# Performance work log

Measured on AMD Instinct MI355X. Metric: run time of the kernel, lower is better.

## Reference

```python
import jax, jax.numpy as jnp
import numpy as np

N_NODES = 50000
N_EDGES = 800000
LN_EPS = 1e-5


def setup_inputs() -> dict:
    key = jax.random.key(0)
    ks = jax.random.split(key, 6)
    B, N, D = 2, N_NODES, 128
    x = jax.random.normal(ks[0], (B, N, D), dtype=jnp.float32)
    A_rows = jax.random.randint(ks[1], (N_EDGES,), 0, N, dtype=jnp.int32)
    A_cols = jax.random.randint(ks[2], (N_EDGES,), 0, N, dtype=jnp.int32)
    A_vals = jax.random.uniform(ks[3], (N_EDGES,), dtype=jnp.float32)
    W = jax.random.normal(ks[4], (D, D), dtype=jnp.float32) * (1.0 / np.sqrt(D))
    b = jnp.zeros((D,), dtype=jnp.float32)
    gamma = jnp.ones((D,), dtype=jnp.float32)
    beta = jnp.zeros((D,), dtype=jnp.float32)
    return {"x": x, "A_rows": A_rows, "A_cols": A_cols, "A_vals": A_vals,
            "W": W, "b": b, "gamma": gamma, "beta": beta}


def reference(x, A_rows, A_cols, A_vals, W, b, gamma, beta):
    B, N, D = x.shape
    # SpMM: A @ x2 where x2 = x.transpose(0,1).reshape(N, B*D)
    x2 = jnp.transpose(x, (1, 0, 2)).reshape(N, B * D)  # [N, B*D]
    msgs = x2[A_cols] * A_vals[:, None]                 # [E, B*D]
    y2 = jax.ops.segment_sum(msgs, A_rows, num_segments=N)  # [N, B*D]
    out = jnp.transpose(y2.reshape(N, B, D), (1, 0, 2))  # [B, N, D]
    # Linear -> LayerNorm -> GELU (dropout = identity in eval)
    h = out @ W + b
    mu = jnp.mean(h, axis=-1, keepdims=True)
    var = jnp.var(h, axis=-1, keepdims=True)
    h = (h - mu) * jax.lax.rsqrt(var + LN_EPS) * gamma + beta
    return jax.nn.gelu(h, approximate=False)
```

## Files before the change

### kernel.cpp

```cpp
#include <hip/hip_runtime.h>
#include <hip/hip_fp16.h>
#include <cstdint>
#include <cstddef>

#define N_NODES 50000
#define N_EDGES 800000
#define D 128
#define M_ROWS (2 * N_NODES)
#define N_TILES (M_ROWS / 16)
#define LN_EPS 1e-5f

typedef __attribute__((ext_vector_type(8))) short bf16x8;
typedef __attribute__((ext_vector_type(4))) float f32x4;

__device__ inline unsigned short bf16_rne(float f) {
  unsigned u = __float_as_uint(f);
  unsigned r = (u + 0x7FFFu + ((u >> 16) & 1u)) >> 16;
  return (unsigned short)r;
}

__global__ __launch_bounds__(256) void k_prep(const float* __restrict__ W,
                                              unsigned short* __restrict__ wt_hi,
                                              unsigned short* __restrict__ wt_lo,
                                              const int* __restrict__ rows,
                                              int* __restrict__ offs) {
  int b = blockIdx.x;
  if (b < 64) {
    int i = b * 256 + threadIdx.x;
    int d = i >> 7, j = i & 127;
    float v = W[i];
    unsigned short hb = bf16_rne(v);
    float rem = v - __uint_as_float((unsigned)hb << 16);
    wt_hi[j * 128 + d] = hb;
    wt_lo[j * 128 + d] = bf16_rne(rem);
  } else {
    int e = (b - 64) * 256 + threadIdx.x;
    if (e < N_EDGES) atomicAdd(&offs[rows[e]], 1);
  }
}

__global__ __launch_bounds__(1024) void k_scan1(int* __restrict__ offs,
                                                int* __restrict__ bsum) {
  __shared__ int s[1024];
  int tid = threadIdx.x;
  int i = blockIdx.x * 1024 + tid;
  int v = (i < N_NODES) ? offs[i] : 0;
  s[tid] = v;
  __syncthreads();
  for (int o = 1; o < 1024; o <<= 1) {
    int t = (tid >= o) ? s[tid - o] : 0;
    __syncthreads();
    s[tid] += t;
    __syncthreads();
  }
  if (i < N_NODES) offs[i] = s[tid] - v;
  if (tid == 1023) bsum[blockIdx.x] = s[tid];
}

__global__ void k_scan2(int* __restrict__ bsum, int nb) {
  if (threadIdx.x == 0) {
    int run = 0;
    for (int b = 0; b < nb; b++) { int t = bsum[b]; bsum[b] = run; run += t; }
  }
}

__global__ __launch_bounds__(1024) void k_scan3(int* __restrict__ offs,
                                                const int* __restrict__ bsum) {
  int i = blockIdx.x * 1024 + threadIdx.x;
  if (i < N_NODES) offs[i] += bsum[blockIdx.x];
}

__global__ __launch_bounds__(256) void k_scatter(const int* __restrict__ rows,
                                                 const int* __restrict__ cols,
                                                 const float* __restrict__ vals,
                                                 int* __restrict__ offs,
                                                 int2* __restrict__ epair) {
  int e = blockIdx.x * 256 + threadIdx.x;
  if (e < N_EDGES) {
    int r = rows[e];
    int pos = atomicAdd(&offs[r], 1);
    int2 p; p.x = cols[e]; p.y = __float_as_int(vals[e]);
    epair[pos] = p;
  }
}

__global__ __launch_bounds__(512) void k_gemm_z(const float* __restrict__ x,
                                                const unsigned short* __restrict__ wt_hi,
                                                const unsigned short* __restrict__ wt_lo,
                                                __half* __restrict__ z) {
  __shared__ unsigned short lw[2][128 * 128];
  int tid = threadIdx.x;

  for (int c = tid; c < 2048; c += 512) {
    int j = c >> 4;
    int k16 = c & 15;
    int soff = j * 256 + ((k16 * 16) ^ ((j & 7) << 4));
    *reinterpret_cast<float4*>(reinterpret_cast<char*>(lw[0]) + soff) =
        *reinterpret_cast<const float4*>(wt_hi + j * 128 + k16 * 8);
    *reinterpret_cast<float4*>(reinterpret_cast<char*>(lw[1]) + soff) =
        *reinterpret_cast<const float4*>(wt_lo + j * 128 + k16 * 8);
  }

  int wave = tid >> 6, l = tid & 63;
  int tile = blockIdx.x * 8 + wave;
  bool active = tile < N_TILES;
  int lrow = l & 15;
  int kg = l >> 4;

  float4 xv[4][2];
  if (active) {
    const float* xr = x + (size_t)(tile * 16 + lrow) * D + kg * 8;
#pragma unroll
    for (int kc = 0; kc < 4; kc++) {
      xv[kc][0] = *reinterpret_cast<const float4*>(xr + kc * 32);
      xv[kc][1] = *reinterpret_cast<const float4*>(xr + kc * 32 + 4);
    }
  } else {
#pragma unroll
    for (int kc = 0; kc < 4; kc++) {
      xv[kc][0] = float4{0.f, 0.f, 0.f, 0.f};
      xv[kc][1] = float4{0.f, 0.f, 0.f, 0.f};
    }
  }
  __syncthreads();

  bf16x8 ahi[4], alo[4];
#pragma unroll
  for (int kc = 0; kc < 4; kc++) {
    float tmp[8];
    *reinterpret_cast<float4*>(&tmp[0]) = xv[kc][0];
    *reinterpret_cast<float4*>(&tmp[4]) = xv[kc][1];
    bf16x8 h, lo8;
#pragma unroll
    for (int e = 0; e < 8; e++) {
      unsigned short hb = bf16_rne(tmp[e]);
      float rem = tmp[e] - __uint_as_float((unsigned)hb << 16);
      h[e] = (short)hb;
      lo8[e] = (short)bf16_rne(rem);
    }
    ahi[kc] = h; alo[kc] = lo8;
  }

  f32x4 acc[8];
#pragma unroll
  for (int jt = 0; jt < 8; jt++) acc[jt] = (f32x4){0.f, 0.f, 0.f, 0.f};

#pragma unroll
  for (int kc = 0; kc < 4; kc++) {
#pragma unroll
    for (int jt = 0; jt < 8; jt++) {
      int j = jt * 16 + lrow;
      int kbyte = kc * 64 + kg * 16;
      int soff = j * 256 + (kbyte ^ ((j & 7) << 4));
      bf16x8 bhi = *reinterpret_cast<bf16x8*>(reinterpret_cast<char*>(lw[0]) + soff);
      bf16x8 blo = *reinterpret_cast<bf16x8*>(reinterpret_cast<char*>(lw[1]) + soff);
      acc[jt] = __builtin_amdgcn_mfma_f32_16x16x32_bf16(ahi[kc], bhi, acc[jt], 0, 0, 0);
      acc[jt] = __builtin_amdgcn_mfma_f32_16x16x32_bf16(alo[kc], bhi, acc[jt], 0, 0, 0);
      acc[jt] = __builtin_amdgcn_mfma_f32_16x16x32_bf16(ahi[kc], blo, acc[jt], 0, 0, 0);
    }
  }

  __syncthreads();
  unsigned short* lds = &lw[0][0] + (size_t)wave * 2176;
  int rbase = kg * 4;
#pragma unroll
  for (int jt = 0; jt < 8; jt++) {
#pragma unroll
    for (int r = 0; r < 4; r++) {
      __half hv = __float2half(acc[jt][r]);
      lds[(rbase + r) * 136 + jt * 16 + lrow] = __half_as_ushort(hv);
    }
  }
  __syncthreads();
  if (active) {
    const char* ldsb = reinterpret_cast<const char*>(lds);
#pragma unroll
    for (int r = 0; r < 16; r++) {
      unsigned v = *reinterpret_cast<const unsigned*>(ldsb + r * 272 + 4 * l);
      *reinterpret_cast<unsigned*>(&z[(size_t)(tile * 16 + r) * D + 2 * l]) = v;
    }
  }
}

__device__ inline float gelu_exact(float v) {
  return 0.5f * v * (1.0f + erff(v * 0.70710678118654752440f));
}

__global__ __launch_bounds__(256) void k_spmm_ln(const __half* __restrict__ z,
                                                 const int* __restrict__ offs,
                                                 const int2* __restrict__ epair,
                                                 const float* __restrict__ bias,
                                                 const float* __restrict__ gamma,
                                                 const float* __restrict__ beta,
                                                 float* __restrict__ out) {
  int r = blockIdx.x * 4 + (threadIdx.x >> 6);
  int l = threadIdx.x & 63;
  int start = (r == 0) ? 0 : offs[r - 1];
  int end = offs[r];

  float2 a0 = {0.f, 0.f}, a1 = {0.f, 0.f};
  const __half* z1 = z + (size_t)N_NODES * D;

  int k = start;
  for (; k + 1 < end; k += 2) {
    int2 e0 = epair[k];
    int2 e1 = epair[k + 1];
    size_t b0 = (size_t)e0.x * D + 2 * l;
    size_t b1 = (size_t)e1.x * D + 2 * l;
    float v0 = __int_as_float(e0.y);
    float v1 = __int_as_float(e1.y);
    float2 f00 = __half22float2(*reinterpret_cast<const __half2*>(&z[b0]));
    float2 f01 = __half22float2(*reinterpret_cast<const __half2*>(&z1[b0]));
    float2 f10 = __half22float2(*reinterpret_cast<const __half2*>(&z[b1]));
    float2 f11 = __half22float2(*reinterpret_cast<const __half2*>(&z1[b1]));
    a0.x += v0 * f00.x; a0.y += v0 * f00.y;
    a1.x += v0 * f01.x; a1.y += v0 * f01.y;
    a0.x += v1 * f10.x; a0.y += v1 * f10.y;
    a1.x += v1 * f11.x; a1.y += v1 * f11.y;
  }
  if (k < end) {
    int2 e0 = epair[k];
    size_t b0 = (size_t)e0.x * D + 2 * l;
    float v0 = __int_as_float(e0.y);
    float2 f00 = __half22float2(*reinterpret_cast<const __half2*>(&z[b0]));
    float2 f01 = __half22float2(*reinterpret_cast<const __half2*>(&z1[b0]));
    a0.x += v0 * f00.x; a0.y += v0 * f00.y;
    a1.x += v0 * f01.x; a1.y += v0 * f01.y;
  }

  float2 bv = *reinterpret_cast<const float2*>(&bias[2 * l]);
  float2 gv = *reinterpret_cast<const float2*>(&gamma[2 * l]);
  float2 ev = *reinterpret_cast<const float2*>(&beta[2 * l]);

  float h0x = a0.x + bv.x, h0y = a0.y + bv.y;
  float h1x = a1.x + bv.x, h1y = a1.y + bv.y;

  float s0 = h0x + h0y, q0 = h0x * h0x + h0y * h0y;
  float s1 = h1x + h1y, q1 = h1x * h1x + h1y * h1y;
#pragma unroll
  for (int off = 32; off >= 1; off >>= 1) {
    s0 += __shfl_xor(s0, off, 64);
    q0 += __shfl_xor(q0, off, 64);
    s1 += __shfl_xor(s1, off, 64);
    q1 += __shfl_xor(q1, off, 64);
  }
  float mu0 = s0 * (1.0f / 128.0f);
  float var0 = q0 * (1.0f / 128.0f) - mu0 * mu0;
  float inv0 = rsqrtf(var0 + LN_EPS);
  float mu1 = s1 * (1.0f / 128.0f);
  float var1 = q1 * (1.0f / 128.0f) - mu1 * mu1;
  float inv1 = rsqrtf(var1 + LN_EPS);

  float2 o0, o1;
  o0.x = gelu_exact((h0x - mu0) * inv0 * gv.x + ev.x);
  o0.y = gelu_exact((h0y - mu0) * inv0 * gv.y + ev.y);
  o1.x = gelu_exact((h1x - mu1) * inv1 * gv.x + ev.x);
  o1.y = gelu_exact((h1y - mu1) * inv1 * gv.y + ev.y);

  *reinterpret_cast<float2*>(&out[(size_t)r * D + 2 * l]) = o0;
  *reinterpret_cast<float2*>(&out[((size_t)N_NODES + r) * D + 2 * l]) = o1;
}

extern "C" void kernel_launch(void* const* d_in, const int* in_sizes, int n_in,
                              void* d_out, int out_size, void* d_ws, size_t ws_size,
                              hipStream_t stream) {
  const float* x      = (const float*)d_in[0];
  const int*   A_rows = (const int*)d_in[1];
  const int*   A_cols = (const int*)d_in[2];
  const float* A_vals = (const float*)d_in[3];
  const float* W      = (const float*)d_in[4];
  const float* b      = (const float*)d_in[5];
  const float* gamma  = (const float*)d_in[6];
  const float* beta   = (const float*)d_in[7];
  float* out = (float*)d_out;

  char* ws = (char*)d_ws;
  size_t off = 0;
  auto alloc = [&](size_t bytes) {
    char* p = ws + off;
    off += (bytes + 255) & ~(size_t)255;
    return p;
  };
  __half*         zbuf  = (__half*)alloc((size_t)M_ROWS * D * sizeof(__half));
  int*            offs  = (int*)alloc((size_t)N_NODES * sizeof(int));
  int*            bsum  = (int*)alloc(4096);
  int2*           epair = (int2*)alloc((size_t)N_EDGES * sizeof(int2));
  unsigned short* wt_hi = (unsigned short*)alloc(128 * 128 * sizeof(unsigned short));
  unsigned short* wt_lo = (unsigned short*)alloc(128 * 128 * sizeof(unsigned short));

  const int nb = (N_NODES + 1023) / 1024;

  hipMemsetAsync(offs, 0, N_NODES * sizeof(int), stream);

  k_prep<<<64 + (N_EDGES + 255) / 256, 256, 0, stream>>>(W, wt_hi, wt_lo,
                                                         A_rows, offs);
  k_scan1<<<nb, 1024, 0, stream>>>(offs, bsum);
  k_scan2<<<1, 64, 0, stream>>>(bsum, nb);
  k_scan3<<<nb, 1024, 0, stream>>>(offs, bsum);
  k_scatter<<<(N_EDGES + 255) / 256, 256, 0, stream>>>(A_rows, A_cols, A_vals,
                                                       offs, epair);
  k_gemm_z<<<(N_TILES + 7) / 8, 512, 0, stream>>>(x, wt_hi, wt_lo, zbuf);
  k_spmm_ln<<<N_NODES / 4, 256, 0, stream>>>(zbuf, offs, epair, b, gamma, beta, out);
}
```

Measured before the change: 279.4 us.

## Interleave batch rows in z, fuse scatter into GEMM launch, drop scan2

Stores the intermediate z as node-major with both batch halves interleaved in one 512-byte row, so each SpMM gather fetches 8 bytes per lane in one load instead of two separate 4-byte loads. Each half-wave now handles one batch with a 32-lane LayerNorm reduction. The edge scatter is merged into the GEMM launch as extra blocks, and the serial scan2 kernel is replaced by a wave reduction inside scan3. Row counting in k_prep is vectorised with int4 loads. Scatter blocks sit in a kernel that reserves 64KB of LDS, which may limit their occupancy.

```diff
diff --git a/kernel.cpp b/kernel.cpp
--- a/kernel.cpp
+++ b/kernel.cpp
@@ -8,6 +8,9 @@
 #define D 128
 #define M_ROWS (2 * N_NODES)
 #define N_TILES (M_ROWS / 16)
+#define TILES_PER_BATCH (N_NODES / 16)
+#define GEMM_BLOCKS ((N_TILES + 7) / 8)
+#define SCAT_BLOCKS ((N_EDGES + 511) / 512)
 #define LN_EPS 1e-5f
 
 typedef __attribute__((ext_vector_type(8))) short bf16x8;
@@ -34,8 +37,16 @@
     wt_hi[j * 128 + d] = hb;
     wt_lo[j * 128 + d] = bf16_rne(rem);
   } else {
-    int e = (b - 64) * 256 + threadIdx.x;
-    if (e < N_EDGES) atomicAdd(&offs[rows[e]], 1);
+    int base = (b - 64) * 1024 + threadIdx.x * 4;
+    if (base + 3 < N_EDGES) {
+      int4 rr = *reinterpret_cast<const int4*>(&rows[base]);
+      atomicAdd(&offs[rr.x], 1);
+      atomicAdd(&offs[rr.y], 1);
+      atomicAdd(&offs[rr.z], 1);
+      atomicAdd(&offs[rr.w], 1);
+    } else {
+      for (int e = base; e < N_EDGES; e++) atomicAdd(&offs[rows[e]], 1);
+    }
   }
 }
 
@@ -57,40 +68,44 @@
   if (tid == 1023) bsum[blockIdx.x] = s[tid];
 }
 
-__global__ void k_scan2(int* __restrict__ bsum, int nb) {
-  if (threadIdx.x == 0) {
-    int run = 0;
-    for (int b = 0; b < nb; b++) { int t = bsum[b]; bsum[b] = run; run += t; }
-  }
-}
-
 __global__ __launch_bounds__(1024) void k_scan3(int* __restrict__ offs,
                                                 const int* __restrict__ bsum) {
-  int i = blockIdx.x * 1024 + threadIdx.x;
-  if (i < N_NODES) offs[i] += bsum[blockIdx.x];
-}
-
-__global__ __launch_bounds__(256) void k_scatter(const int* __restrict__ rows,
-                                                 const int* __restrict__ cols,
-                                                 const float* __restrict__ vals,
-                                                 int* __restrict__ offs,
-                                                 int2* __restrict__ epair) {
-  int e = blockIdx.x * 256 + threadIdx.x;
-  if (e < N_EDGES) {
-    int r = rows[e];
-    int pos = atomicAdd(&offs[r], 1);
-    int2 p; p.x = cols[e]; p.y = __float_as_int(vals[e]);
-    epair[pos] = p;
-  }
-}
-
-__global__ __launch_bounds__(512) void k_gemm_z(const float* __restrict__ x,
-                                                const unsigned short* __restrict__ wt_hi,
-                                                const unsigned short* __restrict__ wt_lo,
-                                                __half* __restrict__ z) {
+  __shared__ int spfx;
+  int tid = threadIdx.x, bid = blockIdx.x;
+  if (tid < 64) {
+    int v = (tid < bid) ? bsum[tid] : 0;
+#pragma unroll
+    for (int o = 32; o >= 1; o >>= 1) v += __shfl_xor(v, o, 64);
+    if (tid == 0) spfx = v;
+  }
+  __syncthreads();
+  int i = bid * 1024 + tid;
+  if (i < N_NODES) offs[i] += spfx;
+}
+
+__global__ __launch_bounds__(512) void k_gemm_scatter(
+    const float* __restrict__ x,
+    const unsigned short* __restrict__ wt_hi,
+    const unsigned short* __restrict__ wt_lo,
+    __half* __restrict__ z,
+    const int* __restrict__ rows,
+    const int* __restrict__ cols,
+    const float* __restrict__ vals,
+    int* __restrict__ offs,
+    int2* __restrict__ epair) {
   __shared__ unsigned short lw[2][128 * 128];
+  if (blockIdx.x >= GEMM_BLOCKS) {
+    int e = (blockIdx.x - GEMM_BLOCKS) * 512 + threadIdx.x;
+    if (e < N_EDGES) {
+      int r = rows[e];
+      int pos = atomicAdd(&offs[r], 1);
+      int2 p; p.x = cols[e]; p.y = __float_as_int(vals[e]);
+      epair[pos] = p;
+    }
+    return;
+  }
+
   int tid = threadIdx.x;
-
   for (int c = tid; c < 2048; c += 512) {
     int j = c >> 4;
     int k16 = c & 15;
@@ -173,11 +188,14 @@
   }
   __syncthreads();
   if (active) {
+    int bb = (tile >= TILES_PER_BATCH);
+    int n0 = tile * 16 - bb * N_NODES;
     const char* ldsb = reinterpret_cast<const char*>(lds);
+    char* zb = reinterpret_cast<char*>(z);
 #pragma unroll
     for (int r = 0; r < 16; r++) {
       unsigned v = *reinterpret_cast<const unsigned*>(ldsb + r * 272 + 4 * l);
-      *reinterpret_cast<unsigned*>(&z[(size_t)(tile * 16 + r) * D + 2 * l]) = v;
+      *reinterpret_cast<unsigned*>(zb + (size_t)(n0 + r) * 512 + bb * 256 + 4 * l) = v;
     }
   }
 }
@@ -198,67 +216,76 @@
   int start = (r == 0) ? 0 : offs[r - 1];
   int end = offs[r];
 
-  float2 a0 = {0.f, 0.f}, a1 = {0.f, 0.f};
-  const __half* z1 = z + (size_t)N_NODES * D;
+  const char* zc = reinterpret_cast<const char*>(z);
+  float4 acc = {0.f, 0.f, 0.f, 0.f};
 
   int k = start;
-  for (; k + 1 < end; k += 2) {
+  for (; k + 3 < end; k += 4) {
     int2 e0 = epair[k];
     int2 e1 = epair[k + 1];
-    size_t b0 = (size_t)e0.x * D + 2 * l;
-    size_t b1 = (size_t)e1.x * D + 2 * l;
+    int2 e2 = epair[k + 2];
+    int2 e3 = epair[k + 3];
+    uint2 p0 = *reinterpret_cast<const uint2*>(zc + (size_t)e0.x * 512 + 8 * l);
+    uint2 p1 = *reinterpret_cast<const uint2*>(zc + (size_t)e1.x * 512 + 8 * l);
+    uint2 p2 = *reinterpret_cast<const uint2*>(zc + (size_t)e2.x * 512 + 8 * l);
+    uint2 p3 = *reinterpret_cast<const uint2*>(zc + (size_t)e3.x * 512 + 8 * l);
+    float v0 = __int_as_float(e0.y), v1 = __int_as_float(e1.y);
+    float v2 = __int_as_float(e2.y), v3 = __int_as_float(e3.y);
+    {
+      float2 lo = __half22float2(*reinterpret_cast<const __half2*>(&p0.x));
+      float2 hi = __half22float2(*reinterpret_cast<const __half2*>(&p0.y));
+      acc.x += v0 * lo.x; acc.y += v0 * lo.y; acc.z += v0 * hi.x; acc.w += v0 * hi.y;
+    }
+    {
+      float2 lo = __half22float2(*reinterpret_cast<const __half2*>(&p1.x));
+      float2 hi = __half22float2(*reinterpret_cast<const __half2*>(&p1.y));
+      acc.x += v1 * lo.x; acc.y += v1 * lo.y; acc.z += v1 * hi.x; acc.w += v1 * hi.y;
+    }
+    {
+      float2 lo = __half22float2(*reinterpret_cast<const __half2*>(&p2.x));
+      float2 hi = __half22float2(*reinterpret_cast<const __half2*>(&p2.y));
+      acc.x += v2 * lo.x; acc.y += v2 * lo.y; acc.z += v2 * hi.x; acc.w += v2 * hi.y;
+    }
+    {
+      float2 lo = __half22float2(*reinterpret_cast<const __half2*>(&p3.x));
+      float2 hi = __half22float2(*reinterpret_cast<const __half2*>(&p3.y));
+      acc.x += v3 * lo.x; acc.y += v3 * lo.y; acc.z += v3 * hi.x; acc.w += v3 * hi.y;
+    }
+  }
+  for (; k < end; k++) {
+    int2 e0 = epair[k];
+    uint2 p0 = *reinterpret_cast<const uint2*>(zc + (size_t)e0.x * 512 + 8 * l);
     float v0 = __int_as_float(e0.y);
-    float v1 = __int_as_float(e1.y);
-    float2 f00 = __half22float2(*reinterpret_cast<const __half2*>(&z[b0]));
-    float2 f01 = __half22float2(*reinterpret_cast<const __half2*>(&z1[b0]));
-    float2 f10 = __half22float2(*reinterpret_cast<const __half2*>(&z[b1]));
-    float2 f11 = __half22float2(*reinterpret_cast<const __half2*>(&z1[b1]));
-    a0.x += v0 * f00.x; a0.y += v0 * f00.y;
-    a1.x += v0 * f01.x; a1.y += v0 * f01.y;
-    a0.x += v1 * f10.x; a0.y += v1 * f10.y;
-    a1.x += v1 * f11.x; a1.y += v1 * f11.y;
-  }
-  if (k < end) {
-    int2 e0 = epair[k];
-    size_t b0 = (size_t)e0.x * D + 2 * l;
-    float v0 = __int_as_float(e0.y);
-    float2 f00 = __half22float2(*reinterpret_cast<const __half2*>(&z[b0]));
-    float2 f01 = __half22float2(*reinterpret_cast<const __half2*>(&z1[b0]));
-    a0.x += v0 * f00.x; a0.y += v0 * f00.y;
-    a1.x += v0 * f01.x; a1.y += v0 * f01.y;
-  }
-
-  float2 bv = *reinterpret_cast<const float2*>(&bias[2 * l]);
-  float2 gv = *reinterpret_cast<const float2*>(&gamma[2 * l]);
-  float2 ev = *reinterpret_cast<const float2*>(&beta[2 * l]);
-
-  float h0x = a0.x + bv.x, h0y = a0.y + bv.y;
-  float h1x = a1.x + bv.x, h1y = a1.y + bv.y;
-
-  float s0 = h0x + h0y, q0 = h0x * h0x + h0y * h0y;
-  float s1 = h1x + h1y, q1 = h1x * h1x + h1y * h1y;
-#pragma unroll
-  for (int off = 32; off >= 1; off >>= 1) {
-    s0 += __shfl_xor(s0, off, 64);
-    q0 += __shfl_xor(q0, off, 64);
-    s1 += __shfl_xor(s1, off, 64);
-    q1 += __shfl_xor(q1, off, 64);
-  }
-  float mu0 = s0 * (1.0f / 128.0f);
-  float var0 = q0 * (1.0f / 128.0f) - mu0 * mu0;
-  float inv0 = rsqrtf(var0 + LN_EPS);
-  float mu1 = s1 * (1.0f / 128.0f);
-  float var1 = q1 * (1.0f / 128.0f) - mu1 * mu1;
-  float inv1 = rsqrtf(var1 + LN_EPS);
-
-  float2 o0, o1;
-  o0.x = gelu_exact((h0x - mu0) * inv0 * gv.x + ev.x);
-  o0.y = gelu_exact((h0y - mu0) * inv0 * gv.y + ev.y);
-  o1.x = gelu_exact((h1x - mu1) * inv1 * gv.x + ev.x);
-  o1.y = gelu_exact((h1y - mu1) * inv1 * gv.y + ev.y);
-
-  *reinterpret_cast<float2*>(&out[(size_t)r * D + 2 * l]) = o0;
-  *reinterpret_cast<float2*>(&out[((size_t)N_NODES + r) * D + 2 * l]) = o1;
+    float2 lo = __half22float2(*reinterpret_cast<const __half2*>(&p0.x));
+    float2 hi = __half22float2(*reinterpret_cast<const __half2*>(&p0.y));
+    acc.x += v0 * lo.x; acc.y += v0 * lo.y; acc.z += v0 * hi.x; acc.w += v0 * hi.y;
+  }
+
+  int p = l >> 5;
+  int j0 = (l & 31) * 4;
+  float4 bv = *reinterpret_cast<const float4*>(&bias[j0]);
+  float4 gv = *reinterpret_cast<const float4*>(&gamma[j0]);
+  float4 ev = *reinterpret_cast<const float4*>(&beta[j0]);
+
+  float h0 = acc.x + bv.x, h1 = acc.y + bv.y, h2 = acc.z + bv.z, h3 = acc.w + bv.w;
+  float s = h0 + h1 + h2 + h3;
+  float q = h0 * h0 + h1 * h1 + h2 * h2 + h3 * h3;
+#pragma unroll
+  for (int o = 16; o >= 1; o >>= 1) {
+    s += __shfl_xor(s, o, 64);
+    q += __shfl_xor(q, o, 64);
+  }
+  float mu = s * (1.0f / 128.0f);
+  float var = q * (1.0f / 128.0f) - mu * mu;
+  float inv = rsqrtf(var + LN_EPS);
+
+  float4 o4;
+  o4.x = gelu_exact((h0 - mu) * inv * gv.x + ev.x);
+  o4.y = gelu_exact((h1 - mu) * inv * gv.y + ev.y);
+  o4.z = gelu_exact((h2 - mu) * inv * gv.z + ev.z);
+  o4.w = gelu_exact((h3 - mu) * inv * gv.w + ev.w);
+
+  *reinterpret_cast<float4*>(&out[(size_t)p * N_NODES * D + (size_t)r * D + j0]) = o4;
 }
 
 extern "C" void kernel_launch(void* const* d_in, const int* in_sizes, int n_in,
@@ -292,13 +319,11 @@
 
   hipMemsetAsync(offs, 0, N_NODES * sizeof(int), stream);
 
-  k_prep<<<64 + (N_EDGES + 255) / 256, 256, 0, stream>>>(W, wt_hi, wt_lo,
-                                                         A_rows, offs);
+  k_prep<<<64 + (N_EDGES / 4 + 255) / 256, 256, 0, stream>>>(W, wt_hi, wt_lo,
+                                                             A_rows, offs);
   k_scan1<<<nb, 1024, 0, stream>>>(offs, bsum);
-  k_scan2<<<1, 64, 0, stream>>>(bsum, nb);
   k_scan3<<<nb, 1024, 0, stream>>>(offs, bsum);
-  k_scatter<<<(N_EDGES + 255) / 256, 256, 0, stream>>>(A_rows, A_cols, A_vals,
-                                                       offs, epair);
-  k_gemm_z<<<(N_TILES + 7) / 8, 512, 0, stream>>>(x, wt_hi, wt_lo, zbuf);
+  k_gemm_scatter<<<GEMM_BLOCKS + SCAT_BLOCKS, 512, 0, stream>>>(
+      x, wt_hi, wt_lo, zbuf, A_rows, A_cols, A_vals, offs, epair);
   k_spmm_ln<<<N_NODES / 4, 256, 0, stream>>>(zbuf, offs, epair, b, gamma, beta, out);
 }
```

Result: faster. 273.2 us (-2.2%).
